# Optimization experiments

Hardware: AMD Instinct MI355X
Metric: run time of the kernel (lower is better)

Reference implementation:

```python
import jax, jax.numpy as jnp
import numpy as np

SHAPE = (160, 160, 160)  # spatial grid (D, H, W)
N_VOX = 400_000
C_IN, C_OUT, K = 32, 64, 3


def setup_inputs() -> dict:
    key = jax.random.key(0)
    k1, k2, k3 = jax.random.split(key, 3)
    # unique active voxel coords (batch=0, z, y, x)
    rng = np.random.default_rng(0)
    flat = rng.choice(SHAPE[0] * SHAPE[1] * SHAPE[2], size=N_VOX, replace=False)
    z, y, x = np.unravel_index(flat, SHAPE)
    coors = np.stack([np.zeros(N_VOX, np.int32), z.astype(np.int32), y.astype(np.int32), x.astype(np.int32)], axis=1)
    features = jax.random.normal(k1, (N_VOX, C_IN), dtype=jnp.float32)
    weight = jax.random.normal(k2, (K * K * K, C_IN, C_OUT), dtype=jnp.float32) * (1.0 / np.sqrt(C_IN * K * K * K))
    bias = jax.random.normal(k3, (C_OUT,), dtype=jnp.float32) * 0.01
    return {"features": features, "coors": jnp.asarray(coors), "weight": weight, "bias": bias, "batch_size": 1}


def reference(features, coors, weight, bias, batch_size):
    # Submanifold sparse 3D conv: output coords == input coords.
    n = features.shape[0]
    b, z, y, x = coors[:, 0], coors[:, 1], coors[:, 2], coors[:, 3]
    D, H, W = SHAPE
    # dense voxel->row index lookup grid (the "hash map" for rulebook build)
    grid = jnp.full((batch_size, D, H, W), -1, dtype=jnp.int32)
    grid = grid.at[b, z, y, x].set(jnp.arange(n, dtype=jnp.int32))
    out = jnp.broadcast_to(bias, (n, C_OUT)).astype(features.dtype)
    k = 0
    for dz in (-1, 0, 1):
        for dy in (-1, 0, 1):
            for dx in (-1, 0, 1):
                nz, ny, nx = z + dz, y + dy, x + dx
                inb = (nz >= 0) & (nz < D) & (ny >= 0) & (ny < H) & (nx >= 0) & (nx < W)
                idx = grid[b, jnp.clip(nz, 0, D - 1), jnp.clip(ny, 0, H - 1), jnp.clip(nx, 0, W - 1)]
                valid = inb & (idx >= 0)
                gathered = jnp.where(valid[:, None], features[jnp.clip(idx, 0)], 0.0)  # [n, C_IN]
                out = out + gathered @ weight[k]  # small GEMM per kernel offset
                k += 1
    return out
```

## Files before the change

### kernel.cpp

```cpp
#include <hip/hip_runtime.h>
#include <stdint.h>

#define DD 160
#define HH 160
#define WW 160
#define NGRID (DD*HH*WW)
#define CIN 32
#define COUT 64
#define KK 27
#define BLOCK 1024
#define WPB 16
#define NBLOCKS 256
#define M27 0x07FFFFFFu

typedef _Float16 h2_t __attribute__((ext_vector_type(2)));

__device__ __forceinline__ h2_t as_h2(uint32_t u) {
    union { uint32_t u; h2_t h; } c; c.u = u; return c.h;
}
__device__ __forceinline__ uint32_t f2h(float f) {
    union { _Float16 h; uint16_t u; } c; c.h = (_Float16)f; return (uint32_t)c.u;
}

__device__ __forceinline__ float dot2(uint32_t fu, uint32_t wu, float acc) {
#if defined(__has_builtin)
#if __has_builtin(__builtin_amdgcn_fdot2)
    return __builtin_amdgcn_fdot2(as_h2(fu), as_h2(wu), acc, false);
#else
    h2_t f = as_h2(fu), w = as_h2(wu);
    acc = fmaf((float)f.x, (float)w.x, acc);
    return fmaf((float)f.y, (float)w.y, acc);
#endif
#else
    h2_t f = as_h2(fu), w = as_h2(wu);
    acc = fmaf((float)f.x, (float)w.x, acc);
    return fmaf((float)f.y, (float)w.y, acc);
#endif
}

__global__ void scatter_grid(const int4* __restrict__ coors, int* __restrict__ grid, int n) {
    int i = blockIdx.x * 256 + threadIdx.x;
    if (i < n) {
        int4 c = coors[i];
        grid[(c.y*HH + c.z)*WW + c.w] = i;
    }
}

__global__ void pack_weights(const float* __restrict__ w, uint4* __restrict__ wpk) {
    int t = blockIdx.x * 256 + threadIdx.x;
    if (t >= KK*4*COUT) return;
    int co = t & 63;
    int g  = (t >> 6) & 3;
    int k  = t >> 8;
    const float* base = w + (size_t)k*CIN*COUT + (size_t)(8*g)*COUT + co;
    uint4 r;
    r.x = f2h(base[0*COUT]) | (f2h(base[1*COUT]) << 16);
    r.y = f2h(base[2*COUT]) | (f2h(base[3*COUT]) << 16);
    r.z = f2h(base[4*COUT]) | (f2h(base[5*COUT]) << 16);
    r.w = f2h(base[6*COUT]) | (f2h(base[7*COUT]) << 16);
    wpk[t] = r;
}

__global__ void feats_to_h(const float4* __restrict__ f, uint2* __restrict__ o, int nq) {
    int i = blockIdx.x * 256 + threadIdx.x;
    if (i < nq) {
        float4 v = f[i];
        uint2 r;
        r.x = f2h(v.x) | (f2h(v.y) << 16);
        r.y = f2h(v.z) | (f2h(v.w) << 16);
        o[i] = r;
    }
}

#define LOAD4(D0,D1,D2,D3,kk) { \
    int j_ = __builtin_amdgcn_readlane(nidx, base + (kk)); \
    const uint4* fp_ = fh4 + (size_t)j_ * 4; \
    D0 = fp_[0]; D1 = fp_[1]; D2 = fp_[2]; D3 = fp_[3]; }

#define MAC4(F0,F1,F2,F3,kk) { \
    const uint4* wl_ = wlds + (size_t)(kk)*4*COUT + lane; \
    uint4 w0_ = wl_[0], w1_ = wl_[COUT], w2_ = wl_[2*COUT], w3_ = wl_[3*COUT]; \
    a0 = dot2(F0.x, w0_.x, a0); a1 = dot2(F0.y, w0_.y, a1); \
    a2 = dot2(F0.z, w0_.z, a2); a3 = dot2(F0.w, w0_.w, a3); \
    a0 = dot2(F1.x, w1_.x, a0); a1 = dot2(F1.y, w1_.y, a1); \
    a2 = dot2(F1.z, w1_.z, a2); a3 = dot2(F1.w, w1_.w, a3); \
    a0 = dot2(F2.x, w2_.x, a0); a1 = dot2(F2.y, w2_.y, a1); \
    a2 = dot2(F2.z, w2_.z, a2); a3 = dot2(F2.w, w2_.w, a3); \
    a0 = dot2(F3.x, w3_.x, a0); a1 = dot2(F3.y, w3_.y, a1); \
    a2 = dot2(F3.z, w3_.z, a2); a3 = dot2(F3.w, w3_.w, a3); }

__global__ __launch_bounds__(BLOCK, 4) void sparse_conv(
    const uint4* __restrict__ fh4, const int4* __restrict__ cc,
    const float* __restrict__ bias, const uint4* __restrict__ wpk,
    const int* __restrict__ grid, float* __restrict__ out, int n)
{
    extern __shared__ uint4 wlds[];

    for (int t = threadIdx.x; t < KK*4*COUT; t += BLOCK)
        wlds[t] = wpk[t];
    __syncthreads();

    const int lane = threadIdx.x & 63;
    const int wave = __builtin_amdgcn_readfirstlane((int)(threadIdx.x >> 6));
    const int stride = NBLOCKS * WPB;
    const int pairstep = 2 * stride;

    const float b = bias[lane];
    const int pl = lane & 31;
    const bool prober = pl < KK;
    const int dz = pl / 9 - 1;
    const int dy = (pl / 3) % 3 - 1;
    const int dx = pl % 3 - 1;
    const int hioff = (lane >= 32) ? stride : 0;

    int v = blockIdx.x * WPB + wave;
    int nidx = -1;

    auto probe = [&](int pb) -> int {
        int r = -1;
        int pv = pb + hioff;
        if (prober && pv < n) {
            int4 c = cc[pv];
            int nz = c.y + dz, ny = c.z + dy, nx = c.w + dx;
            if (nz >= 0 && nz < DD && ny >= 0 && ny < HH && nx >= 0 && nx < WW)
                r = grid[(nz*HH + ny)*WW + nx];
        }
        return r;
    };

    auto runvox = [&](uint32_t m, int base, int vo) {
        float a0 = 0.f, a1 = 0.f, a2 = 0.f, a3 = 0.f;
        uint4 A0, A1, A2, A3, B0, B1, B2, B3;
        int kA = __ffs(m) - 1; m &= m - 1;
        LOAD4(A0, A1, A2, A3, kA);
        for (;;) {
            if (!m) { MAC4(A0, A1, A2, A3, kA); break; }
            int kB = __ffs(m) - 1; m &= m - 1;
            LOAD4(B0, B1, B2, B3, kB);
            MAC4(A0, A1, A2, A3, kA);
            if (!m) { MAC4(B0, B1, B2, B3, kB); break; }
            kA = __ffs(m) - 1; m &= m - 1;
            LOAD4(A0, A1, A2, A3, kA);
            MAC4(B0, B1, B2, B3, kB);
        }
        float r = b + ((a0 + a1) + (a2 + a3));
        __builtin_nontemporal_store(r, out + (size_t)vo * COUT + lane);
    };

    nidx = probe(v);

    while (v < n) {
        unsigned long long bal = __ballot(nidx >= 0);
        int nidx_next = probe(v + pairstep);

        uint32_t m0 = (uint32_t)bal & M27;
        uint32_t m1 = (uint32_t)(bal >> 32) & M27;

        {
            int saved = nidx;
            runvox(m0, 0, v);
            int vB = v + stride;
            if (vB < n) runvox(m1, 32, vB);
            nidx = saved;
        }

        v += pairstep;
        nidx = nidx_next;
    }
}

extern "C" void kernel_launch(void* const* d_in, const int* in_sizes, int n_in,
                              void* d_out, int out_size, void* d_ws, size_t ws_size,
                              hipStream_t stream) {
    const float* feats  = (const float*)d_in[0];
    const int*   coors  = (const int*)d_in[1];
    const float* weight = (const float*)d_in[2];
    const float* bias   = (const float*)d_in[3];
    float*       outp   = (float*)d_out;

    const int n = in_sizes[1] / 4;

    int*   grid = (int*)d_ws;
    uint4* wpk  = (uint4*)((char*)d_ws + (size_t)NGRID * sizeof(int));
    uint2* fh   = (uint2*)((char*)d_ws + (size_t)NGRID * sizeof(int)
                           + (size_t)KK * 4 * COUT * sizeof(uint4));

    hipMemsetAsync(grid, 0xFF, (size_t)NGRID * sizeof(int), stream);
    scatter_grid<<<(n + 255) / 256, 256, 0, stream>>>((const int4*)coors, grid, n);

    pack_weights<<<(KK*4*COUT + 255) / 256, 256, 0, stream>>>(weight, wpk);
    feats_to_h<<<(n * CIN / 4 + 255) / 256, 256, 0, stream>>>((const float4*)feats, fh, n * CIN / 4);

    const size_t lds = (size_t)KK * 4 * COUT * sizeof(uint4);
    sparse_conv<<<NBLOCKS, BLOCK, lds, stream>>>((const uint4*)fh, (const int4*)coors,
                                                 bias, wpk, grid, outp, n);
}
```

Measured before the change: 319.6 us.

## Fuse prep kernels and split output channels across block pairs

Merges the grid scatter, weight packing and feature fp16 conversion into one prep kernel, and adds a zero row so missing neighbours read zeros instead of branching. The conv kernel now launches twice as many blocks, each covering half of the output channels with half the LDS weights. Each wave handles two voxels at once, one per half-wave, over the union of their neighbour masks. This cuts launch overhead and per-wave divergence and raises occupancy. The cost is that each gathered feature row is now loaded by two blocks, and union masks add wasted loads of the zero row.

```diff
diff --git a/kernel.cpp b/kernel.cpp
--- a/kernel.cpp
+++ b/kernel.cpp
@@ -10,7 +10,9 @@
 #define KK 27
 #define BLOCK 1024
 #define WPB 16
-#define NBLOCKS 256
+#define NSLICE 256
+#define PAIR 4096
+#define STEP 8192
 #define M27 0x07FFFFFFu
 
 typedef _Float16 h2_t __attribute__((ext_vector_type(2)));
@@ -38,48 +40,54 @@
 #endif
 }
 
-__global__ void scatter_grid(const int4* __restrict__ coors, int* __restrict__ grid, int n) {
-    int i = blockIdx.x * 256 + threadIdx.x;
-    if (i < n) {
-        int4 c = coors[i];
-        grid[(c.y*HH + c.z)*WW + c.w] = i;
-    }
-}
-
-__global__ void pack_weights(const float* __restrict__ w, uint4* __restrict__ wpk) {
-    int t = blockIdx.x * 256 + threadIdx.x;
-    if (t >= KK*4*COUT) return;
-    int co = t & 63;
-    int g  = (t >> 6) & 3;
-    int k  = t >> 8;
-    const float* base = w + (size_t)k*CIN*COUT + (size_t)(8*g)*COUT + co;
-    uint4 r;
-    r.x = f2h(base[0*COUT]) | (f2h(base[1*COUT]) << 16);
-    r.y = f2h(base[2*COUT]) | (f2h(base[3*COUT]) << 16);
-    r.z = f2h(base[4*COUT]) | (f2h(base[5*COUT]) << 16);
-    r.w = f2h(base[6*COUT]) | (f2h(base[7*COUT]) << 16);
-    wpk[t] = r;
-}
-
-__global__ void feats_to_h(const float4* __restrict__ f, uint2* __restrict__ o, int nq) {
-    int i = blockIdx.x * 256 + threadIdx.x;
-    if (i < nq) {
-        float4 v = f[i];
+__global__ void prep(const float4* __restrict__ f4, const int4* __restrict__ coors,
+                     const float* __restrict__ w, uint2* __restrict__ fh,
+                     int* __restrict__ grid, uint4* __restrict__ wpk, int n)
+{
+    int gid = blockIdx.x * 256 + threadIdx.x;
+    const int nq = n * 8;
+    if (gid < nq) {
+        float4 v = f4[gid];
         uint2 r;
         r.x = f2h(v.x) | (f2h(v.y) << 16);
         r.y = f2h(v.z) | (f2h(v.w) << 16);
-        o[i] = r;
+        fh[gid] = r;
+    } else if (gid < nq + 8) {
+        uint2 z; z.x = 0u; z.y = 0u;
+        fh[gid] = z;
+    } else if (gid < nq + 8 + n) {
+        int i = gid - (nq + 8);
+        int4 c = coors[i];
+        grid[(c.y*HH + c.z)*WW + c.w] = i;
+    } else if (gid < nq + 8 + n + KK*4*COUT) {
+        int t = gid - (nq + 8 + n);
+        int co = t & 63;
+        int g  = (t >> 6) & 3;
+        int k  = t >> 8;
+        const float* base = w + (size_t)k*CIN*COUT + (size_t)(8*g)*COUT + co;
+        uint4 r;
+        r.x = f2h(base[0*COUT]) | (f2h(base[1*COUT]) << 16);
+        r.y = f2h(base[2*COUT]) | (f2h(base[3*COUT]) << 16);
+        r.z = f2h(base[4*COUT]) | (f2h(base[5*COUT]) << 16);
+        r.w = f2h(base[6*COUT]) | (f2h(base[7*COUT]) << 16);
+        wpk[t] = r;
     }
 }
 
-#define LOAD4(D0,D1,D2,D3,kk) { \
-    int j_ = __builtin_amdgcn_readlane(nidx, base + (kk)); \
-    const uint4* fp_ = fh4 + (size_t)j_ * 4; \
+#define RESOLVE(kk, JV) { \
+    int iA_ = __builtin_amdgcn_readlane(nidx, (kk)); \
+    int iB_ = __builtin_amdgcn_readlane(nidx, (kk) + 32); \
+    iA_ = (iA_ < 0) ? n : iA_; \
+    iB_ = (iB_ < 0) ? n : iB_; \
+    JV = lolane ? iA_ : iB_; }
+
+#define LOAD4(D0,D1,D2,D3,JV) { \
+    const uint4* fp_ = fh4 + (size_t)(JV) * 4; \
     D0 = fp_[0]; D1 = fp_[1]; D2 = fp_[2]; D3 = fp_[3]; }
 
 #define MAC4(F0,F1,F2,F3,kk) { \
-    const uint4* wl_ = wlds + (size_t)(kk)*4*COUT + lane; \
-    uint4 w0_ = wl_[0], w1_ = wl_[COUT], w2_ = wl_[2*COUT], w3_ = wl_[3*COUT]; \
+    const uint4* wl_ = wlds + (size_t)(kk)*128 + co; \
+    uint4 w0_ = wl_[0], w1_ = wl_[32], w2_ = wl_[64], w3_ = wl_[96]; \
     a0 = dot2(F0.x, w0_.x, a0); a1 = dot2(F0.y, w0_.y, a1); \
     a2 = dot2(F0.z, w0_.z, a2); a3 = dot2(F0.w, w0_.w, a3); \
     a0 = dot2(F1.x, w1_.x, a0); a1 = dot2(F1.y, w1_.y, a1); \
@@ -89,31 +97,36 @@
     a0 = dot2(F3.x, w3_.x, a0); a1 = dot2(F3.y, w3_.y, a1); \
     a2 = dot2(F3.z, w3_.z, a2); a3 = dot2(F3.w, w3_.w, a3); }
 
-__global__ __launch_bounds__(BLOCK, 4) void sparse_conv(
+__global__ __launch_bounds__(BLOCK, 8) void sparse_conv(
     const uint4* __restrict__ fh4, const int4* __restrict__ cc,
     const float* __restrict__ bias, const uint4* __restrict__ wpk,
     const int* __restrict__ grid, float* __restrict__ out, int n)
 {
-    extern __shared__ uint4 wlds[];
-
-    for (int t = threadIdx.x; t < KK*4*COUT; t += BLOCK)
-        wlds[t] = wpk[t];
+    __shared__ uint4 wlds[KK*4*32];
+
+    const int h  = blockIdx.x & 1;
+    const int sb = blockIdx.x >> 1;
+
+    for (int t = threadIdx.x; t < KK*4*32; t += BLOCK) {
+        int k = t >> 7, g = (t >> 5) & 3, c = t & 31;
+        wlds[t] = wpk[(k*4 + g)*COUT + h*32 + c];
+    }
     __syncthreads();
 
     const int lane = threadIdx.x & 63;
     const int wave = __builtin_amdgcn_readfirstlane((int)(threadIdx.x >> 6));
-    const int stride = NBLOCKS * WPB;
-    const int pairstep = 2 * stride;
-
-    const float b = bias[lane];
-    const int pl = lane & 31;
+    const bool lolane = lane < 32;
+    const int co = lane & 31;
+    const float b = bias[h*32 + co];
+
+    const int pl = co;
     const bool prober = pl < KK;
     const int dz = pl / 9 - 1;
     const int dy = (pl / 3) % 3 - 1;
     const int dx = pl % 3 - 1;
-    const int hioff = (lane >= 32) ? stride : 0;
-
-    int v = blockIdx.x * WPB + wave;
+    const int hioff = lolane ? 0 : PAIR;
+
+    int v = sb * WPB + wave;
     int nidx = -1;
 
     auto probe = [&](int pb) -> int {
@@ -128,43 +141,39 @@
         return r;
     };
 
-    auto runvox = [&](uint32_t m, int base, int vo) {
+    nidx = probe(v);
+
+    while (v < n) {
+        unsigned long long bal = __ballot(nidx >= 0);
+        int nidx_next = probe(v + STEP);
+
+        uint32_t mA = (uint32_t)bal & M27;
+        uint32_t mB = (uint32_t)(bal >> 32) & M27;
+        uint32_t m  = mA | mB;
+
         float a0 = 0.f, a1 = 0.f, a2 = 0.f, a3 = 0.f;
         uint4 A0, A1, A2, A3, B0, B1, B2, B3;
+        int jA, jB;
         int kA = __ffs(m) - 1; m &= m - 1;
-        LOAD4(A0, A1, A2, A3, kA);
+        RESOLVE(kA, jA); LOAD4(A0, A1, A2, A3, jA);
         for (;;) {
             if (!m) { MAC4(A0, A1, A2, A3, kA); break; }
             int kB = __ffs(m) - 1; m &= m - 1;
-            LOAD4(B0, B1, B2, B3, kB);
+            RESOLVE(kB, jB); LOAD4(B0, B1, B2, B3, jB);
             MAC4(A0, A1, A2, A3, kA);
             if (!m) { MAC4(B0, B1, B2, B3, kB); break; }
             kA = __ffs(m) - 1; m &= m - 1;
-            LOAD4(A0, A1, A2, A3, kA);
+            RESOLVE(kA, jA); LOAD4(A0, A1, A2, A3, jA);
             MAC4(B0, B1, B2, B3, kB);
         }
+
         float r = b + ((a0 + a1) + (a2 + a3));
-        __builtin_nontemporal_store(r, out + (size_t)vo * COUT + lane);
-    };
-
-    nidx = probe(v);
-
-    while (v < n) {
-        unsigned long long bal = __ballot(nidx >= 0);
-        int nidx_next = probe(v + pairstep);
-
-        uint32_t m0 = (uint32_t)bal & M27;
-        uint32_t m1 = (uint32_t)(bal >> 32) & M27;
-
-        {
-            int saved = nidx;
-            runvox(m0, 0, v);
-            int vB = v + stride;
-            if (vB < n) runvox(m1, 32, vB);
-            nidx = saved;
-        }
-
-        v += pairstep;
+        int vB = v + PAIR;
+        int vo = lolane ? v : vB;
+        if (lolane || vB < n)
+            __builtin_nontemporal_store(r, out + (size_t)vo * COUT + h*32 + co);
+
+        v += STEP;
         nidx = nidx_next;
     }
 }
@@ -186,12 +195,11 @@
                            + (size_t)KK * 4 * COUT * sizeof(uint4));
 
     hipMemsetAsync(grid, 0xFF, (size_t)NGRID * sizeof(int), stream);
-    scatter_grid<<<(n + 255) / 256, 256, 0, stream>>>((const int4*)coors, grid, n);
-
-    pack_weights<<<(KK*4*COUT + 255) / 256, 256, 0, stream>>>(weight, wpk);
-    feats_to_h<<<(n * CIN / 4 + 255) / 256, 256, 0, stream>>>((const float4*)feats, fh, n * CIN / 4);
-
-    const size_t lds = (size_t)KK * 4 * COUT * sizeof(uint4);
-    sparse_conv<<<NBLOCKS, BLOCK, lds, stream>>>((const uint4*)fh, (const int4*)coors,
-                                                 bias, wpk, grid, outp, n);
-}
+
+    const int prep_total = n*8 + 8 + n + KK*4*COUT;
+    prep<<<(prep_total + 255) / 256, 256, 0, stream>>>(
+        (const float4*)feats, (const int4*)coors, weight, fh, grid, wpk, n);
+
+    sparse_conv<<<NSLICE*2, BLOCK, 0, stream>>>((const uint4*)fh, (const int4*)coors,
+                                                bias, wpk, grid, outp, n);
+}
```

New measurement: 1.101 ms. 3.44x slower.

## Merge prep kernels and pipeline gathers across both voxels of a pair

Applied to the files above, without the earlier changes.

The three preprocessing kernels (feature fp16 conversion, grid scatter, weight packing) are fused into one launch to cut launch overhead. The main loop stops processing the two voxels of a wave pair one after the other. It now pops neighbor jobs from both masks into a single triple-buffered stream of gather loads, with two accumulator sets and sched_barriers keeping the loads in flight ahead of the MACs. The aim is to hide gather latency across voxel boundaries, at the cost of more live registers and branchy job selection.

```diff
diff --git a/kernel.cpp b/kernel.cpp
--- a/kernel.cpp
+++ b/kernel.cpp
@@ -11,6 +11,8 @@
 #define BLOCK 1024
 #define WPB 16
 #define NBLOCKS 256
+#define PAIR 4096
+#define STEP 8192
 #define M27 0x07FFFFFFu
 
 typedef _Float16 h2_t __attribute__((ext_vector_type(2)));
@@ -38,46 +40,48 @@
 #endif
 }
 
-__global__ void scatter_grid(const int4* __restrict__ coors, int* __restrict__ grid, int n) {
-    int i = blockIdx.x * 256 + threadIdx.x;
-    if (i < n) {
-        int4 c = coors[i];
-        grid[(c.y*HH + c.z)*WW + c.w] = i;
-    }
-}
-
-__global__ void pack_weights(const float* __restrict__ w, uint4* __restrict__ wpk) {
-    int t = blockIdx.x * 256 + threadIdx.x;
-    if (t >= KK*4*COUT) return;
-    int co = t & 63;
-    int g  = (t >> 6) & 3;
-    int k  = t >> 8;
-    const float* base = w + (size_t)k*CIN*COUT + (size_t)(8*g)*COUT + co;
-    uint4 r;
-    r.x = f2h(base[0*COUT]) | (f2h(base[1*COUT]) << 16);
-    r.y = f2h(base[2*COUT]) | (f2h(base[3*COUT]) << 16);
-    r.z = f2h(base[4*COUT]) | (f2h(base[5*COUT]) << 16);
-    r.w = f2h(base[6*COUT]) | (f2h(base[7*COUT]) << 16);
-    wpk[t] = r;
-}
-
-__global__ void feats_to_h(const float4* __restrict__ f, uint2* __restrict__ o, int nq) {
-    int i = blockIdx.x * 256 + threadIdx.x;
-    if (i < nq) {
-        float4 v = f[i];
+__global__ void prep(const float4* __restrict__ f4, const int4* __restrict__ coors,
+                     const float* __restrict__ w, uint2* __restrict__ fh,
+                     int* __restrict__ grid, uint4* __restrict__ wpk, int n)
+{
+    int gid = blockIdx.x * 256 + threadIdx.x;
+    const int nq = n * 8;
+    if (gid < nq) {
+        float4 v = f4[gid];
         uint2 r;
         r.x = f2h(v.x) | (f2h(v.y) << 16);
         r.y = f2h(v.z) | (f2h(v.w) << 16);
-        o[i] = r;
+        fh[gid] = r;
+    } else if (gid < nq + n) {
+        int i = gid - nq;
+        int4 c = coors[i];
+        grid[(c.y*HH + c.z)*WW + c.w] = i;
+    } else if (gid < nq + n + KK*4*COUT) {
+        int t = gid - (nq + n);
+        int co = t & 63;
+        int g  = (t >> 6) & 3;
+        int k  = t >> 8;
+        const float* base = w + (size_t)k*CIN*COUT + (size_t)(8*g)*COUT + co;
+        uint4 r;
+        r.x = f2h(base[0*COUT]) | (f2h(base[1*COUT]) << 16);
+        r.y = f2h(base[2*COUT]) | (f2h(base[3*COUT]) << 16);
+        r.z = f2h(base[4*COUT]) | (f2h(base[5*COUT]) << 16);
+        r.w = f2h(base[6*COUT]) | (f2h(base[7*COUT]) << 16);
+        wpk[t] = r;
     }
 }
 
-#define LOAD4(D0,D1,D2,D3,kk) { \
-    int j_ = __builtin_amdgcn_readlane(nidx, base + (kk)); \
+#define POP(K,S,H) { \
+    if (mlo)      { K = __ffs(mlo) - 1; mlo &= mlo - 1; S = 0; H = true; } \
+    else if (mhi) { K = __ffs(mhi) - 1; mhi &= mhi - 1; S = 1; H = true; } \
+    else H = false; }
+
+#define LOADJOB(D0,D1,D2,D3,K,S) { \
+    int j_ = __builtin_amdgcn_readlane(nidx, (K) + ((S) ? 32 : 0)); \
     const uint4* fp_ = fh4 + (size_t)j_ * 4; \
     D0 = fp_[0]; D1 = fp_[1]; D2 = fp_[2]; D3 = fp_[3]; }
 
-#define MAC4(F0,F1,F2,F3,kk) { \
+#define MAC4(F0,F1,F2,F3,kk,a0,a1,a2,a3) { \
     const uint4* wl_ = wlds + (size_t)(kk)*4*COUT + lane; \
     uint4 w0_ = wl_[0], w1_ = wl_[COUT], w2_ = wl_[2*COUT], w3_ = wl_[3*COUT]; \
     a0 = dot2(F0.x, w0_.x, a0); a1 = dot2(F0.y, w0_.y, a1); \
@@ -89,6 +93,10 @@
     a0 = dot2(F3.x, w3_.x, a0); a1 = dot2(F3.y, w3_.y, a1); \
     a2 = dot2(F3.z, w3_.z, a2); a3 = dot2(F3.w, w3_.w, a3); }
 
+#define MACJOB(F0,F1,F2,F3,K,S) { \
+    if ((S) == 0) { MAC4(F0,F1,F2,F3,K,aA0,aA1,aA2,aA3) } \
+    else          { MAC4(F0,F1,F2,F3,K,aB0,aB1,aB2,aB3) } }
+
 __global__ __launch_bounds__(BLOCK, 4) void sparse_conv(
     const uint4* __restrict__ fh4, const int4* __restrict__ cc,
     const float* __restrict__ bias, const uint4* __restrict__ wpk,
@@ -102,8 +110,6 @@
 
     const int lane = threadIdx.x & 63;
     const int wave = __builtin_amdgcn_readfirstlane((int)(threadIdx.x >> 6));
-    const int stride = NBLOCKS * WPB;
-    const int pairstep = 2 * stride;
 
     const float b = bias[lane];
     const int pl = lane & 31;
@@ -111,7 +117,7 @@
     const int dz = pl / 9 - 1;
     const int dy = (pl / 3) % 3 - 1;
     const int dx = pl % 3 - 1;
-    const int hioff = (lane >= 32) ? stride : 0;
+    const int hioff = (lane >= 32) ? PAIR : 0;
 
     int v = blockIdx.x * WPB + wave;
     int nidx = -1;
@@ -128,43 +134,55 @@
         return r;
     };
 
-    auto runvox = [&](uint32_t m, int base, int vo) {
-        float a0 = 0.f, a1 = 0.f, a2 = 0.f, a3 = 0.f;
-        uint4 A0, A1, A2, A3, B0, B1, B2, B3;
-        int kA = __ffs(m) - 1; m &= m - 1;
-        LOAD4(A0, A1, A2, A3, kA);
-        for (;;) {
-            if (!m) { MAC4(A0, A1, A2, A3, kA); break; }
-            int kB = __ffs(m) - 1; m &= m - 1;
-            LOAD4(B0, B1, B2, B3, kB);
-            MAC4(A0, A1, A2, A3, kA);
-            if (!m) { MAC4(B0, B1, B2, B3, kB); break; }
-            kA = __ffs(m) - 1; m &= m - 1;
-            LOAD4(A0, A1, A2, A3, kA);
-            MAC4(B0, B1, B2, B3, kB);
-        }
-        float r = b + ((a0 + a1) + (a2 + a3));
-        __builtin_nontemporal_store(r, out + (size_t)vo * COUT + lane);
-    };
-
     nidx = probe(v);
 
     while (v < n) {
         unsigned long long bal = __ballot(nidx >= 0);
-        int nidx_next = probe(v + pairstep);
-
-        uint32_t m0 = (uint32_t)bal & M27;
-        uint32_t m1 = (uint32_t)(bal >> 32) & M27;
-
-        {
-            int saved = nidx;
-            runvox(m0, 0, v);
-            int vB = v + stride;
-            if (vB < n) runvox(m1, 32, vB);
-            nidx = saved;
+        int nidx_next = probe(v + STEP);
+
+        uint32_t mlo = (uint32_t)bal & M27;
+        uint32_t mhi = (uint32_t)(bal >> 32) & M27;
+
+        float aA0 = 0.f, aA1 = 0.f, aA2 = 0.f, aA3 = 0.f;
+        float aB0 = 0.f, aB1 = 0.f, aB2 = 0.f, aB3 = 0.f;
+        uint4 P0, P1, P2, P3, Q0, Q1, Q2, Q3, R0, R1, R2, R3;
+        int kP, sP, kQ, sQ, kR, sR;
+        bool hP, hQ, hR;
+
+        POP(kP, sP, hP);
+        LOADJOB(P0, P1, P2, P3, kP, sP);
+        POP(kQ, sQ, hQ);
+        if (hQ) LOADJOB(Q0, Q1, Q2, Q3, kQ, sQ);
+        POP(kR, sR, hR);
+        if (hR) LOADJOB(R0, R1, R2, R3, kR, sR);
+
+        for (;;) {
+            __builtin_amdgcn_sched_barrier(0);
+            MACJOB(P0, P1, P2, P3, kP, sP);
+            if (!hQ) break;
+            POP(kP, sP, hP);
+            if (hP) LOADJOB(P0, P1, P2, P3, kP, sP);
+            __builtin_amdgcn_sched_barrier(0);
+            MACJOB(Q0, Q1, Q2, Q3, kQ, sQ);
+            if (!hR) break;
+            POP(kQ, sQ, hQ);
+            if (hQ) LOADJOB(Q0, Q1, Q2, Q3, kQ, sQ);
+            __builtin_amdgcn_sched_barrier(0);
+            MACJOB(R0, R1, R2, R3, kR, sR);
+            if (!hP) break;
+            POP(kR, sR, hR);
+            if (hR) LOADJOB(R0, R1, R2, R3, kR, sR);
         }
 
-        v += pairstep;
+        float rA = b + ((aA0 + aA1) + (aA2 + aA3));
+        __builtin_nontemporal_store(rA, out + (size_t)v * COUT + lane);
+        int vB = v + PAIR;
+        if (vB < n) {
+            float rB = b + ((aB0 + aB1) + (aB2 + aB3));
+            __builtin_nontemporal_store(rB, out + (size_t)vB * COUT + lane);
+        }
+
+        v += STEP;
         nidx = nidx_next;
     }
 }
@@ -186,10 +204,10 @@
                            + (size_t)KK * 4 * COUT * sizeof(uint4));
 
     hipMemsetAsync(grid, 0xFF, (size_t)NGRID * sizeof(int), stream);
-    scatter_grid<<<(n + 255) / 256, 256, 0, stream>>>((const int4*)coors, grid, n);
-
-    pack_weights<<<(KK*4*COUT + 255) / 256, 256, 0, stream>>>(weight, wpk);
-    feats_to_h<<<(n * CIN / 4 + 255) / 256, 256, 0, stream>>>((const float4*)feats, fh, n * CIN / 4);
+
+    const int prep_total = n*8 + n + KK*4*COUT;
+    prep<<<(prep_total + 255) / 256, 256, 0, stream>>>(
+        (const float4*)feats, (const int4*)coors, weight, fh, grid, wpk, n);
 
     const size_t lds = (size_t)KK * 4 * COUT * sizeof(uint4);
     sparse_conv<<<NBLOCKS, BLOCK, lds, stream>>>((const uint4*)fh, (const int4*)coors,
```

After: 345.7 us. +8.2%, slower.

## Sort voxels spatially by grid order and assign contiguous runs per wave

Applied to the files above, without the earlier changes.

Adds a counting-sort pass: per-1024-cell chunk counts, a single-block scan, and an emit kernel that renumbers active voxels in raster order. It rewrites the grid to the sorted index and converts features to fp16 in that order. The conv kernel now gives each wave a contiguous run of sorted voxels (with block swizzle), so neighbour feature gathers and grid probes hit nearby memory and reuse the cache. In exchange it adds two extra kernel launches, a full 4M-cell grid sweep, atomics, and an indirection through om for output rows.

```diff
diff --git a/kernel.cpp b/kernel.cpp
--- a/kernel.cpp
+++ b/kernel.cpp
@@ -5,12 +5,14 @@
 #define HH 160
 #define WW 160
 #define NGRID (DD*HH*WW)
+#define NCHUNK (NGRID/1024)
 #define CIN 32
 #define COUT 64
 #define KK 27
 #define BLOCK 1024
 #define WPB 16
 #define NBLOCKS 256
+#define TOTW (NBLOCKS*WPB)
 #define M27 0x07FFFFFFu
 
 typedef _Float16 h2_t __attribute__((ext_vector_type(2)));
@@ -38,43 +40,101 @@
 #endif
 }
 
-__global__ void scatter_grid(const int4* __restrict__ coors, int* __restrict__ grid, int n) {
-    int i = blockIdx.x * 256 + threadIdx.x;
-    if (i < n) {
-        int4 c = coors[i];
-        grid[(c.y*HH + c.z)*WW + c.w] = i;
-    }
-}
-
-__global__ void pack_weights(const float* __restrict__ w, uint4* __restrict__ wpk) {
-    int t = blockIdx.x * 256 + threadIdx.x;
-    if (t >= KK*4*COUT) return;
-    int co = t & 63;
-    int g  = (t >> 6) & 3;
-    int k  = t >> 8;
-    const float* base = w + (size_t)k*CIN*COUT + (size_t)(8*g)*COUT + co;
-    uint4 r;
-    r.x = f2h(base[0*COUT]) | (f2h(base[1*COUT]) << 16);
-    r.y = f2h(base[2*COUT]) | (f2h(base[3*COUT]) << 16);
-    r.z = f2h(base[4*COUT]) | (f2h(base[5*COUT]) << 16);
-    r.w = f2h(base[6*COUT]) | (f2h(base[7*COUT]) << 16);
-    wpk[t] = r;
-}
-
-__global__ void feats_to_h(const float4* __restrict__ f, uint2* __restrict__ o, int nq) {
-    int i = blockIdx.x * 256 + threadIdx.x;
-    if (i < nq) {
-        float4 v = f[i];
-        uint2 r;
-        r.x = f2h(v.x) | (f2h(v.y) << 16);
-        r.y = f2h(v.z) | (f2h(v.w) << 16);
-        o[i] = r;
-    }
-}
-
-#define LOAD4(D0,D1,D2,D3,kk) { \
-    int j_ = __builtin_amdgcn_readlane(nidx, base + (kk)); \
-    const uint4* fp_ = fh4 + (size_t)j_ * 4; \
+__global__ void scatter_pack(const int4* __restrict__ coors, const float* __restrict__ w,
+                             int* __restrict__ grid, int* __restrict__ cnt,
+                             uint4* __restrict__ wpk, int n)
+{
+    int gid = blockIdx.x * 256 + threadIdx.x;
+    if (gid < n) {
+        int4 c = coors[gid];
+        int cell = (c.y*HH + c.z)*WW + c.w;
+        grid[cell] = gid;
+        atomicAdd(&cnt[cell >> 10], 1);
+    } else if (gid < n + KK*4*COUT) {
+        int t = gid - n;
+        int co = t & 63;
+        int g  = (t >> 6) & 3;
+        int k  = t >> 8;
+        const float* base = w + (size_t)k*CIN*COUT + (size_t)(8*g)*COUT + co;
+        uint4 r;
+        r.x = f2h(base[0*COUT]) | (f2h(base[1*COUT]) << 16);
+        r.y = f2h(base[2*COUT]) | (f2h(base[3*COUT]) << 16);
+        r.z = f2h(base[4*COUT]) | (f2h(base[5*COUT]) << 16);
+        r.w = f2h(base[6*COUT]) | (f2h(base[7*COUT]) << 16);
+        wpk[t] = r;
+    }
+}
+
+__global__ __launch_bounds__(1024) void scan_chunks(const int* __restrict__ cnt,
+                                                    int* __restrict__ base)
+{
+    __shared__ int s[1024];
+    int t = threadIdx.x;
+    int c0 = 0, c1 = 0, c2 = 0, c3 = 0, sum;
+    int i0 = t * 4;
+    if (i0 + 3 < NCHUNK) { c0 = cnt[i0]; c1 = cnt[i0+1]; c2 = cnt[i0+2]; c3 = cnt[i0+3]; }
+    else {
+        if (i0     < NCHUNK) c0 = cnt[i0];
+        if (i0 + 1 < NCHUNK) c1 = cnt[i0+1];
+        if (i0 + 2 < NCHUNK) c2 = cnt[i0+2];
+        if (i0 + 3 < NCHUNK) c3 = cnt[i0+3];
+    }
+    sum = c0 + c1 + c2 + c3;
+    s[t] = sum; __syncthreads();
+    for (int off = 1; off < 1024; off <<= 1) {
+        int val = (t >= off) ? s[t - off] : 0;
+        __syncthreads();
+        s[t] += val;
+        __syncthreads();
+    }
+    int excl = s[t] - sum;
+    if (i0     < NCHUNK) { base[i0]   = excl; excl += c0; }
+    if (i0 + 1 < NCHUNK) { base[i0+1] = excl; excl += c1; }
+    if (i0 + 2 < NCHUNK) { base[i0+2] = excl; excl += c2; }
+    if (i0 + 3 < NCHUNK) { base[i0+3] = excl; }
+}
+
+__global__ __launch_bounds__(1024) void emit_sort(const float4* __restrict__ f4,
+                                                  int* __restrict__ grid,
+                                                  const int* __restrict__ base,
+                                                  int* __restrict__ pos, int* __restrict__ om,
+                                                  uint2* __restrict__ fh)
+{
+    __shared__ int wt[16];
+    int cell = blockIdx.x * 1024 + threadIdx.x;
+    int g = grid[cell];
+    bool pres = g >= 0;
+    unsigned long long bal = __ballot(pres);
+    int lane = threadIdx.x & 63;
+    int wv = threadIdx.x >> 6;
+    int lpre = __popcll(bal & ((1ull << lane) - 1ull));
+    if (lane == 0) wt[wv] = __popcll(bal);
+    __syncthreads();
+    if (threadIdx.x == 0) {
+        int acc = 0;
+        for (int i = 0; i < 16; ++i) { int c = wt[i]; wt[i] = acc; acc += c; }
+    }
+    __syncthreads();
+    if (pres) {
+        int sp = base[blockIdx.x] + wt[wv] + lpre;
+        pos[sp] = cell;
+        om[sp]  = g;
+        grid[cell] = sp;
+        const float4* src = f4 + (size_t)g * 8;
+        uint2* dst = fh + (size_t)sp * 8;
+        #pragma unroll
+        for (int q = 0; q < 8; ++q) {
+            float4 vv = src[q];
+            uint2 r;
+            r.x = f2h(vv.x) | (f2h(vv.y) << 16);
+            r.y = f2h(vv.z) | (f2h(vv.w) << 16);
+            dst[q] = r;
+        }
+    }
+}
+
+#define LOAD4(D0,D1,D2,D3,J) { \
+    const uint4* fp_ = fh4 + (size_t)(J) * 4; \
     D0 = fp_[0]; D1 = fp_[1]; D2 = fp_[2]; D3 = fp_[3]; }
 
 #define MAC4(F0,F1,F2,F3,kk) { \
@@ -90,9 +150,9 @@
     a2 = dot2(F3.z, w3_.z, a2); a3 = dot2(F3.w, w3_.w, a3); }
 
 __global__ __launch_bounds__(BLOCK, 4) void sparse_conv(
-    const uint4* __restrict__ fh4, const int4* __restrict__ cc,
+    const uint4* __restrict__ fh4, const int* __restrict__ pos, const int* __restrict__ om,
     const float* __restrict__ bias, const uint4* __restrict__ wpk,
-    const int* __restrict__ grid, float* __restrict__ out, int n)
+    const int* __restrict__ grid, float* __restrict__ out, int n, int run)
 {
     extern __shared__ uint4 wlds[];
 
@@ -102,8 +162,11 @@
 
     const int lane = threadIdx.x & 63;
     const int wave = __builtin_amdgcn_readfirstlane((int)(threadIdx.x >> 6));
-    const int stride = NBLOCKS * WPB;
-    const int pairstep = 2 * stride;
+    const int b0 = blockIdx.x;
+    const int sw = ((b0 & 7) << 5) + (b0 >> 3);
+    const int wg = sw * WPB + wave;
+    const int lo = wg * run;
+    const int hi = min(n, lo + run);
 
     const float b = bias[lane];
     const int pl = lane & 31;
@@ -111,60 +174,60 @@
     const int dz = pl / 9 - 1;
     const int dy = (pl / 3) % 3 - 1;
     const int dx = pl % 3 - 1;
-    const int hioff = (lane >= 32) ? stride : 0;
-
-    int v = blockIdx.x * WPB + wave;
+    const int hioff = (lane >= 32) ? 1 : 0;
+
     int nidx = -1;
 
     auto probe = [&](int pb) -> int {
         int r = -1;
         int pv = pb + hioff;
-        if (prober && pv < n) {
-            int4 c = cc[pv];
-            int nz = c.y + dz, ny = c.z + dy, nx = c.w + dx;
+        if (prober && pv < hi) {
+            int cell = pos[pv];
+            int z = cell / (HH*WW); int rem = cell % (HH*WW);
+            int y = rem / WW;       int x = rem % WW;
+            int nz = z + dz, ny = y + dy, nx = x + dx;
             if (nz >= 0 && nz < DD && ny >= 0 && ny < HH && nx >= 0 && nx < WW)
                 r = grid[(nz*HH + ny)*WW + nx];
         }
         return r;
     };
 
-    auto runvox = [&](uint32_t m, int base, int vo) {
+    auto runvox = [&](uint32_t m, int base, int orig) {
         float a0 = 0.f, a1 = 0.f, a2 = 0.f, a3 = 0.f;
         uint4 A0, A1, A2, A3, B0, B1, B2, B3;
         int kA = __ffs(m) - 1; m &= m - 1;
-        LOAD4(A0, A1, A2, A3, kA);
+        int jA = __builtin_amdgcn_readlane(nidx, base + kA);
+        LOAD4(A0, A1, A2, A3, jA);
         for (;;) {
             if (!m) { MAC4(A0, A1, A2, A3, kA); break; }
             int kB = __ffs(m) - 1; m &= m - 1;
-            LOAD4(B0, B1, B2, B3, kB);
+            int jB = __builtin_amdgcn_readlane(nidx, base + kB);
+            LOAD4(B0, B1, B2, B3, jB);
             MAC4(A0, A1, A2, A3, kA);
             if (!m) { MAC4(B0, B1, B2, B3, kB); break; }
             kA = __ffs(m) - 1; m &= m - 1;
-            LOAD4(A0, A1, A2, A3, kA);
+            jA = __builtin_amdgcn_readlane(nidx, base + kA);
+            LOAD4(A0, A1, A2, A3, jA);
             MAC4(B0, B1, B2, B3, kB);
         }
         float r = b + ((a0 + a1) + (a2 + a3));
-        __builtin_nontemporal_store(r, out + (size_t)vo * COUT + lane);
+        __builtin_nontemporal_store(r, out + (size_t)orig * COUT + lane);
     };
 
+    int v = lo;
     nidx = probe(v);
 
-    while (v < n) {
+    while (v < hi) {
         unsigned long long bal = __ballot(nidx >= 0);
-        int nidx_next = probe(v + pairstep);
-
-        uint32_t m0 = (uint32_t)bal & M27;
-        uint32_t m1 = (uint32_t)(bal >> 32) & M27;
-
-        {
-            int saved = nidx;
-            runvox(m0, 0, v);
-            int vB = v + stride;
-            if (vB < n) runvox(m1, 32, vB);
-            nidx = saved;
-        }
-
-        v += pairstep;
+        int nidx_next = probe(v + 2);
+
+        uint32_t mA = (uint32_t)bal & M27;
+        uint32_t mB = (uint32_t)(bal >> 32) & M27;
+
+        runvox(mA, 0, om[v]);
+        if (v + 1 < hi) runvox(mB, 32, om[v + 1]);
+
+        v += 2;
         nidx = nidx_next;
     }
 }
@@ -180,18 +243,27 @@
 
     const int n = in_sizes[1] / 4;
 
-    int*   grid = (int*)d_ws;
-    uint4* wpk  = (uint4*)((char*)d_ws + (size_t)NGRID * sizeof(int));
-    uint2* fh   = (uint2*)((char*)d_ws + (size_t)NGRID * sizeof(int)
-                           + (size_t)KK * 4 * COUT * sizeof(uint4));
-
-    hipMemsetAsync(grid, 0xFF, (size_t)NGRID * sizeof(int), stream);
-    scatter_grid<<<(n + 255) / 256, 256, 0, stream>>>((const int4*)coors, grid, n);
-
-    pack_weights<<<(KK*4*COUT + 255) / 256, 256, 0, stream>>>(weight, wpk);
-    feats_to_h<<<(n * CIN / 4 + 255) / 256, 256, 0, stream>>>((const float4*)feats, fh, n * CIN / 4);
-
+    char* ws = (char*)d_ws;
+    int*   grid = (int*)ws;                                   ws += (size_t)NGRID * 4;
+    int*   cnt  = (int*)ws;                                   ws += (size_t)NCHUNK * 4;
+    int*   base = (int*)ws;                                   ws += (size_t)NCHUNK * 4;
+    uint4* wpk  = (uint4*)ws;                                 ws += (size_t)KK * 4 * COUT * 16;
+    int*   pos  = (int*)ws;                                   ws += (size_t)n * 4;
+    int*   om   = (int*)ws;                                   ws += (size_t)n * 4;
+    uint2* fh   = (uint2*)ws;
+
+    hipMemsetAsync(grid, 0xFF, (size_t)NGRID * 4, stream);
+    hipMemsetAsync(cnt, 0, (size_t)NCHUNK * 4, stream);
+
+    scatter_pack<<<(n + KK*4*COUT + 255) / 256, 256, 0, stream>>>(
+        (const int4*)coors, weight, grid, cnt, wpk, n);
+
+    scan_chunks<<<1, 1024, 0, stream>>>(cnt, base);
+
+    emit_sort<<<NCHUNK, 1024, 0, stream>>>((const float4*)feats, grid, base, pos, om, fh);
+
+    const int run = (n + TOTW - 1) / TOTW;
     const size_t lds = (size_t)KK * 4 * COUT * sizeof(uint4);
-    sparse_conv<<<NBLOCKS, BLOCK, lds, stream>>>((const uint4*)fh, (const int4*)coors,
-                                                 bias, wpk, grid, outp, n);
-}
+    sparse_conv<<<NBLOCKS, BLOCK, lds, stream>>>((const uint4*)fh, pos, om,
+                                                 bias, wpk, grid, outp, n, run);
+}
```

New measurement: 365.3 us. 14.3% more time.
